# Optimization experiments

Measured on AMD Instinct MI355X. Metric: run time of the kernel, lower is better.

Reference implementation:

```python
import jax, jax.numpy as jnp
import numpy as np

L, B, S, D, H, E = 3, 2, 2048, 1024, 16, 4
Dh = D // H  # 64
DF = E * D   # 4096


def _ln(x, g, b, eps=1e-5):
    m = jnp.mean(x, axis=-1, keepdims=True)
    v = jnp.mean(jnp.square(x - m), axis=-1, keepdims=True)
    return (x - m) * jax.lax.rsqrt(v + eps) * g + b


def setup_inputs() -> dict:
    key = jax.random.key(0)
    ks = jax.random.split(key, 12)
    s = 0.02
    f32 = jnp.float32
    return {
        "x":    jax.random.normal(ks[0], (B, S, D), f32),
        "Wq":   jax.random.normal(ks[1], (L, Dh, Dh), f32) * s,
        "Wk":   jax.random.normal(ks[2], (L, Dh, Dh), f32) * s,
        "Wv":   jax.random.normal(ks[3], (L, Dh, Dh), f32) * s,
        "Wo":   jax.random.normal(ks[4], (L, D, D), f32) * s,
        "bo":   jnp.zeros((L, D), f32),
        "ln1_g": jnp.ones((L, D), f32),
        "ln1_b": jnp.zeros((L, D), f32),
        "W1":   jax.random.normal(ks[5], (L, DF, D), f32) * s,
        "b1":   jnp.zeros((L, DF), f32),
        "W2":   jax.random.normal(ks[6], (L, D, DF), f32) * s,
        "b2":   jnp.zeros((L, D), f32),
        "ln2_g": jnp.ones((L, D), f32),
        "ln2_b": jnp.zeros((L, D), f32),
    }


def reference(x, Wq, Wk, Wv, Wo, bo, ln1_g, ln1_b, W1, b1, W2, b2, ln2_g, ln2_b):
    scale = 1.0 / np.sqrt(Dh).astype(np.float32)
    out = x
    for l in range(L):
        xh = out.reshape(B, S, H, Dh)
        # per-head Linear (shared 64x64 weight across heads), torch Linear: y = x @ W.T
        q = jnp.einsum('bshd,ed->bhse', xh, Wq[l])  # [B,H,S,Dh]
        k = jnp.einsum('bshd,ed->bhse', xh, Wk[l])
        v = jnp.einsum('bshd,ed->bhse', xh, Wv[l])
        att = jax.nn.softmax(jnp.einsum('bhse,bhte->bhst', q, k) * scale, axis=-1)
        ctx = jnp.einsum('bhst,bhtd->bshd', att, v).reshape(B, S, D)
        att_out = ctx @ Wo[l].T + bo[l]
        n1 = _ln(att_out + out, ln1_g[l], ln1_b[l])  # residual adds layer input (v == out)
        ff = jax.nn.relu(n1 @ W1[l].T + b1[l]) @ W2[l].T + b2[l]
        out = _ln(ff + n1, ln2_g[l], ln2_b[l])
    return out
```

## Files before the change

kernel.cpp:

```cpp
#include <hip/hip_runtime.h>
#include <hip/hip_bf16.h>
#include <math.h>


#define DEVINL __device__ __forceinline__
typedef unsigned short ushort_t;
using short8 = __attribute__((ext_vector_type(8))) short;
using f32x4  = __attribute__((ext_vector_type(4))) float;

#if defined(__has_builtin)
#if __has_builtin(__builtin_amdgcn_exp2f)
#define EXPFN(x) __builtin_amdgcn_exp2f(x)
#define QSCALE 0.18033688011112042f
#define HAVE_EXP2 1
#endif
#endif
#ifndef HAVE_EXP2
#define EXPFN(x) __expf(x)
#define QSCALE 0.125f
#endif

DEVINL short f2b(float f) {
  unsigned u = __float_as_uint(f);
  u += 0x7fff + ((u >> 16) & 1);
  return (short)(u >> 16);
}
DEVINL unsigned pk2(float a, float b) {
  unsigned ua = __float_as_uint(a), ub = __float_as_uint(b);
  ua += 0x7fff + ((ua >> 16) & 1);
  ub += 0x7fff + ((ub >> 16) & 1);
  return (ua >> 16) | (ub & 0xffff0000u);
}
DEVINL unsigned pkc(float a, float b) {
  float2 f; f.x = a; f.y = b;
  __hip_bfloat162 h = __float22bfloat162_rn(f);
  return *reinterpret_cast<unsigned*>(&h);
}
DEVINL float bl(unsigned u) { return __uint_as_float(u << 16); }
DEVINL float bh(unsigned u) { return __uint_as_float(u & 0xffff0000u); }
DEVINL f32x4 mfma16(short8 a, short8 b, f32x4 c) {
  return __builtin_amdgcn_mfma_f32_16x16x32_bf16(a, b, c, 0, 0, 0);
}

typedef __attribute__((address_space(3))) void lds_void;
typedef __attribute__((address_space(1))) void gbl_void;
DEVINL void gl16(const void* g, void* l) {
  __builtin_amdgcn_global_load_lds((const gbl_void*)(unsigned long long)g,
                                   (lds_void*)(unsigned long long)l, 16, 0, 0);
}
template <int N> DEVINL void waitvm() {
  asm volatile("s_waitcnt vmcnt(%0)" ::"n"(N) : "memory");
}
DEVINL void barrier_raw() { __builtin_amdgcn_s_barrier(); }
DEVINL void sched0() { __builtin_amdgcn_sched_barrier(0); }

__global__ __launch_bounds__(256)
void conv_bf16(const float* __restrict__ src, ushort_t* __restrict__ dst,
               int n8) {
  int i = blockIdx.x * 256 + threadIdx.x;
  const int stride = gridDim.x * 256;
  for (; i < n8; i += stride) {
    float4 a = ((const float4*)src)[2 * i];
    float4 b = ((const float4*)src)[2 * i + 1];
    uint4 o;
    o.x = pk2(a.x, a.y); o.y = pk2(a.z, a.w);
    o.z = pk2(b.x, b.y); o.w = pk2(b.z, b.w);
    ((uint4*)dst)[i] = o;
  }
}

DEVINL float block_sum(float v, float* red) {
#pragma unroll
  for (int off = 32; off > 0; off >>= 1) v += __shfl_xor(v, off, 64);
  if ((threadIdx.x & 63) == 0) red[threadIdx.x >> 6] = v;
  __syncthreads();
  float r = red[0] + red[1] + red[2] + red[3];
  __syncthreads();
  return r;
}

template <bool WF>
__global__ __launch_bounds__(256)
void ln_fuse(const ushort_t* __restrict__ pa, const ushort_t* __restrict__ pb,
             const float* __restrict__ bias, const ushort_t* __restrict__ Rb,
             const float* __restrict__ g, const float* __restrict__ b,
             ushort_t* __restrict__ outb, float* __restrict__ outf) {
  __shared__ float red[4];
  const size_t base = (size_t)blockIdx.x * 1024 + threadIdx.x * 4;
  uint2 ua = *(const uint2*)(pa + base);
  uint2 ub = *(const uint2*)(pb + base);
  uint2 ur = *(const uint2*)(Rb + base);
  float4 vbi = *(const float4*)(bias + threadIdx.x * 4);
  float4 v;
  v.x = bl(ua.x) + bl(ub.x) + bl(ur.x) + vbi.x;
  v.y = bh(ua.x) + bh(ub.x) + bh(ur.x) + vbi.y;
  v.z = bl(ua.y) + bl(ub.y) + bl(ur.y) + vbi.z;
  v.w = bh(ua.y) + bh(ub.y) + bh(ur.y) + vbi.w;
  float s = block_sum(v.x + v.y + v.z + v.w, red);
  float mean = s * (1.0f / 1024.0f);
  float dx = v.x - mean, dy = v.y - mean, dz = v.z - mean, dw = v.w - mean;
  float sq = block_sum(dx * dx + dy * dy + dz * dz + dw * dw, red);
  float rstd = rsqrtf(sq * (1.0f / 1024.0f) + 1e-5f);
  const float4 gv = *(const float4*)(g + threadIdx.x * 4);
  const float4 bv = *(const float4*)(b + threadIdx.x * 4);
  float4 o;
  o.x = dx * rstd * gv.x + bv.x;
  o.y = dy * rstd * gv.y + bv.y;
  o.z = dz * rstd * gv.z + bv.z;
  o.w = dw * rstd * gv.w + bv.w;
  uint2 p;
  p.x = pk2(o.x, o.y); p.y = pk2(o.z, o.w);
  *(uint2*)(outb + base) = p;
  if (WF) *(float4*)(outf + base) = o;
}

template <int BM, int BN, int WR, int WC, bool OBF, int EPI, bool SWZ>
__global__ __launch_bounds__(WR * WC * 64)
void gemm_db(const ushort_t* __restrict__ A, const ushort_t* __restrict__ W,
             const float* __restrict__ bias, void* __restrict__ Cp, int M,
             int N, int Klen, int lda, int ldw) {
  constexpr int THREADS = WR * WC * 64;
  constexpr int FM = BM / WR / 16;
  constexpr int FN = BN / WC / 16;
  constexpr int CA = BM * 8 / THREADS;
  constexpr int CB = BN * 8 / THREADS;
  constexpr int L = CA + CB;
  __shared__ __align__(16) ushort_t As[2][BM * 64];
  __shared__ __align__(16) ushort_t Bs[2][BN * 64];
  const int tid = threadIdx.x;
  const int lane = tid & 63, lo = lane & 15, hi = lane >> 4, w = tid >> 6;
  int bx = blockIdx.x, by = blockIdx.y;
  if (SWZ) {
    int id = by * gridDim.x + bx;
    const int cpx = (gridDim.x * gridDim.y) >> 3;
    id = (id & 7) * cpx + (id >> 3);
    bx = id % gridDim.x;
    by = id / gridDim.x;
  }
  const int m0 = by * BM, n0 = bx * BN;
  const int wm = (w / WC) * (BM / WR), wn = (w % WC) * (BN / WC);
  const int kbase = blockIdx.z * Klen;

  auto stage = [&](int t, int buf) {
    const int k0 = kbase + t * 64;
#pragma unroll
    for (int i = 0; i < CA; ++i) {
      const int c = i * THREADS + tid;
      const int r = c >> 3, sg = (c & 7) ^ (r & 7);
      gl16(A + (size_t)(m0 + r) * lda + k0 + sg * 8, &As[buf][c * 8]);
    }
#pragma unroll
    for (int i = 0; i < CB; ++i) {
      const int c = i * THREADS + tid;
      const int r = c >> 3, sg = (c & 7) ^ (r & 7);
      gl16(W + (size_t)(n0 + r) * ldw + k0 + sg * 8, &Bs[buf][c * 8]);
    }
  };

  f32x4 acc[FM][FN] = {};
  auto compute = [&](int cur) {
#pragma unroll
    for (int ks = 0; ks < 2; ++ks) {
      short8 af[FM], bf_[FN];
#pragma unroll
      for (int fm = 0; fm < FM; ++fm) {
        const int row = wm + fm * 16 + lo;
        af[fm] = *(const short8*)
            &As[cur][row * 64 + (((ks * 4 + hi) ^ (row & 7)) << 3)];
      }
#pragma unroll
      for (int fn = 0; fn < FN; ++fn) {
        const int row = wn + fn * 16 + lo;
        bf_[fn] = *(const short8*)
            &Bs[cur][row * 64 + (((ks * 4 + hi) ^ (row & 7)) << 3)];
      }
#pragma unroll
      for (int fm = 0; fm < FM; ++fm)
#pragma unroll
        for (int fn = 0; fn < FN; ++fn)
          acc[fm][fn] = mfma16(af[fm], bf_[fn], acc[fm][fn]);
    }
  };

  const int nt = Klen / 64;
  stage(0, 0);
  for (int t = 0; t < nt - 1; ++t) {
    const int cur = t & 1;
    stage(t + 1, cur ^ 1);
    waitvm<L>();
    barrier_raw(); sched0();
    compute(cur);
    barrier_raw(); sched0();
  }
  waitvm<0>();
  barrier_raw(); sched0();
  compute((nt - 1) & 1);

  float bv[FN];
#pragma unroll
  for (int fn = 0; fn < FN; ++fn)
    bv[fn] = (EPI & 1) ? bias[n0 + wn + fn * 16 + lo] : 0.f;
#pragma unroll
  for (int fm = 0; fm < FM; ++fm)
#pragma unroll
    for (int fn = 0; fn < FN; ++fn) {
      const int col = n0 + wn + fn * 16 + lo;
#pragma unroll
      for (int r = 0; r < 4; ++r) {
        const int row = m0 + wm + fm * 16 + hi * 4 + r;
        float v = acc[fm][fn][r] + bv[fn];
        if (EPI & 4) v = fmaxf(v, 0.f);
        if (OBF) {
          ushort_t* Cb = (ushort_t*)Cp + (size_t)blockIdx.z * M * N;
          Cb[(size_t)row * N + col] = (ushort_t)f2b(v);
        } else {
          float* Cf = (float*)Cp + (size_t)blockIdx.z * M * N;
          Cf[(size_t)row * N + col] = v;
        }
      }
    }
}

__global__ __launch_bounds__(256)
void qkv_kernel(const ushort_t* __restrict__ A, const ushort_t* __restrict__ Wq,
                const ushort_t* __restrict__ Wk, const ushort_t* __restrict__ Wv,
                ushort_t* __restrict__ q, ushort_t* __restrict__ k,
                ushort_t* __restrict__ v) {
  __shared__ __align__(16) ushort_t As[128 * 64];
  __shared__ __align__(16) ushort_t Ws[3][64 * 64];
  const int tid = threadIdx.x;
  const int lane = tid & 63, lo = lane & 15, hi = lane >> 4, w = tid >> 6;
  const int m0 = blockIdx.x * 128;
  const int wm = (w >> 1) * 64, wn = (w & 1) * 32;

#pragma unroll
  for (int i = 0; i < 4; ++i) {
    const int c = i * 256 + tid;
    const int r = c >> 3, sg = (c & 7) ^ (r & 7);
    gl16(A + (size_t)(m0 + r) * 64 + sg * 8, As + c * 8);
  }
#pragma unroll
  for (int o = 0; o < 3; ++o) {
    const ushort_t* wb = (o == 0) ? Wq : (o == 1) ? Wk : Wv;
#pragma unroll
    for (int i = 0; i < 2; ++i) {
      const int c = i * 256 + tid;
      const int r = c >> 3, sg = (c & 7) ^ (r & 7);
      gl16(wb + (size_t)r * 64 + sg * 8, Ws[o] + c * 8);
    }
  }
  __syncthreads();

#pragma unroll
  for (int o = 0; o < 3; ++o) {
    ushort_t* ob = (o == 0) ? q : (o == 1) ? k : v;
    const float sc = (o == 0) ? QSCALE : 1.0f;
    f32x4 acc[4][2] = {};
#pragma unroll
    for (int ks = 0; ks < 2; ++ks) {
      short8 af[4], bf[2];
#pragma unroll
      for (int fm = 0; fm < 4; ++fm) {
        const int row = wm + fm * 16 + lo;
        af[fm] = *(const short8*)
            &As[row * 64 + (((ks * 4 + hi) ^ (row & 7)) << 3)];
      }
#pragma unroll
      for (int fn = 0; fn < 2; ++fn) {
        const int row = wn + fn * 16 + lo;
        bf[fn] = *(const short8*)
            &Ws[o][row * 64 + (((ks * 4 + hi) ^ (row & 7)) << 3)];
      }
#pragma unroll
      for (int fm = 0; fm < 4; ++fm)
#pragma unroll
        for (int fn = 0; fn < 2; ++fn)
          acc[fm][fn] = mfma16(af[fm], bf[fn], acc[fm][fn]);
    }
#pragma unroll
    for (int fm = 0; fm < 4; ++fm)
#pragma unroll
      for (int fn = 0; fn < 2; ++fn) {
        const int col = wn + fn * 16 + lo;
#pragma unroll
        for (int r = 0; r < 4; ++r) {
          const int row = m0 + wm + fm * 16 + hi * 4 + r;
          size_t idx;
          if (o == 2) {
            idx = (size_t)row * 64 + col;
          } else {
            idx = (size_t)((row >> 15) * 16 + (row & 15)) * 131072 +
                  (size_t)((row >> 4) & 2047) * 64 + col;
          }
          ob[idx] = (ushort_t)f2b(acc[fm][fn][r] * sc);
        }
      }
  }
}

__global__ __launch_bounds__(256)
void vtrans(const ushort_t* __restrict__ V, ushort_t* __restrict__ VT) {
  __shared__ ushort_t T[64][65];
  const int tid = threadIdx.x;
  const int s0 = blockIdx.x * 64, hd0 = blockIdx.y * 64, b = blockIdx.z;
  const ushort_t* src = V + (size_t)b * 2097152;
  ushort_t* dst = VT + (size_t)b * 2097152;
#pragma unroll
  for (int i = 0; i < 2; ++i) {
    int c = tid + i * 256;
    int s = c >> 3, kg = c & 7;
    short8 hv = *(const short8*)(src + (size_t)(s0 + s) * 1024 + hd0 + kg * 8);
#pragma unroll
    for (int j = 0; j < 8; ++j) T[s][kg * 8 + j] = (ushort_t)hv[j];
  }
  __syncthreads();
#pragma unroll
  for (int i = 0; i < 2; ++i) {
    int c = tid + i * 256;
    int hd = c >> 3, sg = c & 7;
    short8 o;
#pragma unroll
    for (int j = 0; j < 8; ++j) o[j] = (short)T[sg * 8 + j][hd];
    *(short8*)(dst + (size_t)(hd0 + hd) * 2048 + s0 + sg * 8) = o;
  }
}

__global__ __launch_bounds__(256)
void attn3(const ushort_t* __restrict__ Qh, const ushort_t* __restrict__ Kh,
           const ushort_t* __restrict__ VT, ushort_t* __restrict__ O) {
  __shared__ __align__(16) ushort_t Kbuf[2][64 * 64];
  __shared__ __align__(16) ushort_t Vbuf[2][64 * 64];
  __shared__ __align__(16) ushort_t Pbuf[4][16 * 40];
  const int tid = threadIdx.x, w = tid >> 6, lane = tid & 63;
  const int lo = lane & 15, hi = lane >> 4;
  const int hid = blockIdx.y * 32 + blockIdx.x;
  const int logical = (hid & 7) * 128 + (hid >> 3);
  const int bh = logical >> 5, qt = logical & 31;
  const int b = bh >> 4, h = bh & 15;
  const size_t hq = (size_t)bh * 131072;
  const size_t vth = (size_t)b * 2097152 + (size_t)h * 131072;
  const size_t oh = (size_t)b * 2097152 + (size_t)h * 64;
  const int qrow = qt * 64 + w * 16;
  ushort_t* Pw = Pbuf[w];

  const ushort_t* qp = Qh + hq + (size_t)(qrow + lo) * 64 + hi * 8;
  const short8 qf0 = *(const short8*)qp;
  const short8 qf1 = *(const short8*)(qp + 32);

  const int c0 = tid, c1 = 256 + tid;
  const int r0 = c0 >> 3, s0 = ((c0 & 7) ^ (r0 & 7)) << 3;
  const int r1 = c1 >> 3, s1 = ((c1 & 7) ^ (r1 & 7)) << 3;
  const ushort_t* kg0 = Kh + hq + (size_t)r0 * 64 + s0;
  const ushort_t* kg1 = Kh + hq + (size_t)r1 * 64 + s1;
  const ushort_t* vg0 = VT + vth + (size_t)r0 * 2048 + s0;
  const ushort_t* vg1 = VT + vth + (size_t)r1 * 2048 + s1;

  auto stage = [&](int kt, int buf) {
    gl16(kg0 + (size_t)kt * 4096, &Kbuf[buf][c0 * 8]);
    gl16(kg1 + (size_t)kt * 4096, &Kbuf[buf][c1 * 8]);
    gl16(vg0 + kt * 64, &Vbuf[buf][c0 * 8]);
    gl16(vg1 + kt * 64, &Vbuf[buf][c1 * 8]);
  };

  f32x4 acc[4] = {};
  f32x4 lacc = {};
  const int sw = lo & 7;
  const int ko0 = (hi ^ sw) << 3, ko1 = ((4 + hi) ^ sw) << 3;

  auto body = [&](const ushort_t* Kc, const ushort_t* Vc) {
    f32x4 sc[4];
#pragma unroll
    for (int fm = 0; fm < 4; ++fm) {
      const int rb = (fm * 16 + lo) * 64;
      f32x4 t = {};
      t = mfma16(*(const short8*)&Kc[rb + ko0], qf0, t);
      t = mfma16(*(const short8*)&Kc[rb + ko1], qf1, t);
      sc[fm] = t;
    }
    short8 vf[4][2];
#pragma unroll
    for (int fn = 0; fn < 4; ++fn) {
      const int rb = (fn * 16 + lo) * 64;
      vf[fn][0] = *(const short8*)&Vc[rb + ko0];
      vf[fn][1] = *(const short8*)&Vc[rb + ko1];
    }
#pragma unroll
    for (int fm = 0; fm < 4; ++fm) {
      f32x4 p;
      p[0] = EXPFN(sc[fm][0]); p[1] = EXPFN(sc[fm][1]);
      p[2] = EXPFN(sc[fm][2]); p[3] = EXPFN(sc[fm][3]);
      lacc += p;
      uint2 pw;
      pw.x = pkc(p[0], p[1]); pw.y = pkc(p[2], p[3]);
      *(uint2*)&Pw[lo * 40 + fm * 16 + hi * 4] = pw;
    }
    short8 pb0 = *(const short8*)&Pw[lo * 40 + hi * 8];
    short8 pb1 = *(const short8*)&Pw[lo * 40 + 32 + hi * 8];
#pragma unroll
    for (int fn = 0; fn < 4; ++fn) {
      acc[fn] = mfma16(vf[fn][0], pb0, acc[fn]);
      acc[fn] = mfma16(vf[fn][1], pb1, acc[fn]);
    }
  };

  stage(0, 0);
  __syncthreads();
  for (int kt2 = 0; kt2 < 16; ++kt2) {
    stage(2 * kt2 + 1, 1);
    body(Kbuf[0], Vbuf[0]);
    __syncthreads();
    if (kt2 < 15) stage(2 * kt2 + 2, 0);
    body(Kbuf[1], Vbuf[1]);
    __syncthreads();
  }

  float lsum = (lacc[0] + lacc[1]) + (lacc[2] + lacc[3]);
  lsum += __shfl_xor(lsum, 16);
  lsum += __shfl_xor(lsum, 32);
  const float inv = 1.0f / lsum;
  ushort_t* op = O + oh + (size_t)(qrow + lo) * 1024 + hi * 4;
#pragma unroll
  for (int fn = 0; fn < 4; ++fn) {
    uint2 o;
    o.x = pk2(acc[fn][0] * inv, acc[fn][1] * inv);
    o.y = pk2(acc[fn][2] * inv, acc[fn][3] * inv);
    *(uint2*)(op + fn * 16) = o;
  }
}

extern "C" void kernel_launch(void* const* d_in, const int* in_sizes, int n_in,
                              void* d_out, int out_size, void* d_ws,
                              size_t ws_size, hipStream_t stream) {
  const float* x    = (const float*)d_in[0];
  const float* Wq   = (const float*)d_in[1];
  const float* Wk   = (const float*)d_in[2];
  const float* Wv   = (const float*)d_in[3];
  const float* Wo   = (const float*)d_in[4];
  const float* bo   = (const float*)d_in[5];
  const float* ln1g = (const float*)d_in[6];
  const float* ln1b = (const float*)d_in[7];
  const float* W1   = (const float*)d_in[8];
  const float* b1   = (const float*)d_in[9];
  const float* W2   = (const float*)d_in[10];
  const float* b2   = (const float*)d_in[11];
  const float* ln2g = (const float*)d_in[12];
  const float* ln2b = (const float*)d_in[13];
  float* out = (float*)d_out;
  char* wsb = (char*)d_ws;

  ushort_t* t0  = (ushort_t*)wsb;
  ushort_t* t0b = t0 + 4194304;
  ushort_t* q   = (ushort_t*)(wsb + (16ull << 20));
  ushort_t* k   = (ushort_t*)(wsb + (24ull << 20));
  ushort_t* v   = (ushort_t*)(wsb + (32ull << 20));
  ushort_t* vt  = (ushort_t*)(wsb + (40ull << 20));
  ushort_t* ff  = q;
  ushort_t* ctx = (ushort_t*)(wsb + (48ull << 20));
  ushort_t* n1b = ctx;
  ushort_t* xbf = (ushort_t*)(wsb + (56ull << 20));
  ushort_t* wqb = (ushort_t*)(wsb + (64ull << 20));
  ushort_t* wkb = wqb + 3 * 4096;
  ushort_t* wvb = wkb + 3 * 4096;
  ushort_t* wob = (ushort_t*)(wsb + (65ull << 20));
  ushort_t* w1b = (ushort_t*)(wsb + (72ull << 20));
  ushort_t* w2b = (ushort_t*)(wsb + (96ull << 20));

  auto conv = [&](const float* s, ushort_t* d, long n) {
    int n8 = (int)(n / 8);
    int g = (n8 + 255) / 256;
    if (g > 2048) g = 2048;
    conv_bf16<<<g, 256, 0, stream>>>(s, d, n8);
  };
  conv(x, xbf, 4194304);
  conv(Wq, wqb, 3 * 4096);
  conv(Wk, wkb, 3 * 4096);
  conv(Wv, wvb, 3 * 4096);
  conv(Wo, wob, 3ll * 1048576);
  conv(W1, w1b, 3ll * 4194304);
  conv(W2, w2b, 3ll * 4194304);

  const ushort_t* curb = xbf;
  for (int l = 0; l < 3; ++l) {
    qkv_kernel<<<512, 256, 0, stream>>>(curb, wqb + l * 4096, wkb + l * 4096,
                                        wvb + l * 4096, q, k, v);
    vtrans<<<dim3(32, 16, 2), 256, 0, stream>>>(v, vt);
    attn3<<<dim3(32, 32), 256, 0, stream>>>(q, k, vt, ctx);
    gemm_db<128, 64, 2, 2, true, 0, true>
        <<<dim3(16, 32, 2), 256, 0, stream>>>(ctx, wob + (size_t)l * 1048576,
                                              nullptr, t0, 4096, 1024, 512,
                                              1024, 1024);
    ln_fuse<false><<<4096, 256, 0, stream>>>(t0, t0b, bo + l * 1024, curb,
                                             ln1g + l * 1024, ln1b + l * 1024,
                                             n1b, nullptr);
    gemm_db<128, 128, 2, 4, true, 5, true>
        <<<dim3(32, 32, 1), 512, 0, stream>>>(n1b, w1b + (size_t)l * 4194304,
                                              b1 + l * 4096, ff, 4096, 4096,
                                              1024, 1024, 1024);
    gemm_db<128, 64, 2, 2, true, 0, true>
        <<<dim3(16, 32, 2), 256, 0, stream>>>(ff, w2b + (size_t)l * 4194304,
                                              nullptr, t0, 4096, 1024, 2048,
                                              4096, 4096);
    if (l == 2)
      ln_fuse<true><<<4096, 256, 0, stream>>>(t0, t0b, b2 + l * 1024, n1b,
                                              ln2g + l * 1024, ln2b + l * 1024,
                                              xbf, out);
    else
      ln_fuse<false><<<4096, 256, 0, stream>>>(t0, t0b, b2 + l * 1024, n1b,
                                               ln2g + l * 1024, ln2b + l * 1024,
                                               xbf, nullptr);
    curb = xbf;
  }
}
```

Before: 611.8 us.

## Double attention query rows per warp and enlarge GEMM tiles

The attention kernel now processes 32 query rows per warp (128 per block) instead of 16, so each K/V tile loaded into LDS and each K fragment read serves two query blocks, halving K/V traffic per query. The grid shrinks to 16x32 blocks. The output-projection and FFN2 GEMMs switch to 128x128 tiles, and the FFN1 GEMM drops to a 2x2 warp layout with 256 threads. More accumulators per warp raise register pressure and fewer blocks may reduce occupancy.

Result: faster. 541.2 us (-11.5%).

```diff
diff --git a/kernel.cpp b/kernel.cpp
--- a/kernel.cpp
+++ b/kernel.cpp
@@ -326,26 +326,29 @@
 }
 
 __global__ __launch_bounds__(256)
-void attn3(const ushort_t* __restrict__ Qh, const ushort_t* __restrict__ Kh,
+void attn4(const ushort_t* __restrict__ Qh, const ushort_t* __restrict__ Kh,
            const ushort_t* __restrict__ VT, ushort_t* __restrict__ O) {
   __shared__ __align__(16) ushort_t Kbuf[2][64 * 64];
   __shared__ __align__(16) ushort_t Vbuf[2][64 * 64];
-  __shared__ __align__(16) ushort_t Pbuf[4][16 * 40];
+  __shared__ __align__(16) ushort_t Pbuf[4][2][16 * 40];
   const int tid = threadIdx.x, w = tid >> 6, lane = tid & 63;
   const int lo = lane & 15, hi = lane >> 4;
-  const int hid = blockIdx.y * 32 + blockIdx.x;
-  const int logical = (hid & 7) * 128 + (hid >> 3);
-  const int bh = logical >> 5, qt = logical & 31;
+  const int hid = blockIdx.y * 16 + blockIdx.x;
+  const int logical = (hid & 7) * 64 + (hid >> 3);
+  const int bh = logical >> 4, qt = logical & 15;
   const int b = bh >> 4, h = bh & 15;
   const size_t hq = (size_t)bh * 131072;
   const size_t vth = (size_t)b * 2097152 + (size_t)h * 131072;
   const size_t oh = (size_t)b * 2097152 + (size_t)h * 64;
-  const int qrow = qt * 64 + w * 16;
-  ushort_t* Pw = Pbuf[w];
-
-  const ushort_t* qp = Qh + hq + (size_t)(qrow + lo) * 64 + hi * 8;
-  const short8 qf0 = *(const short8*)qp;
-  const short8 qf1 = *(const short8*)(qp + 32);
+  const int qrow = qt * 128 + w * 32;
+  ushort_t* Pa = Pbuf[w][0];
+  ushort_t* Pb = Pbuf[w][1];
+
+  const ushort_t* qpa = Qh + hq + (size_t)(qrow + lo) * 64 + hi * 8;
+  const short8 qf0a = *(const short8*)qpa;
+  const short8 qf1a = *(const short8*)(qpa + 32);
+  const short8 qf0b = *(const short8*)(qpa + 1024);
+  const short8 qf1b = *(const short8*)(qpa + 1024 + 32);
 
   const int c0 = tid, c1 = 256 + tid;
   const int r0 = c0 >> 3, s0 = ((c0 & 7) ^ (r0 & 7)) << 3;
@@ -362,20 +365,26 @@
     gl16(vg1 + kt * 64, &Vbuf[buf][c1 * 8]);
   };
 
-  f32x4 acc[4] = {};
-  f32x4 lacc = {};
+  f32x4 acca[4] = {}, accb[4] = {};
+  f32x4 la = {}, lb = {};
   const int sw = lo & 7;
   const int ko0 = (hi ^ sw) << 3, ko1 = ((4 + hi) ^ sw) << 3;
 
   auto body = [&](const ushort_t* Kc, const ushort_t* Vc) {
-    f32x4 sc[4];
+    f32x4 sa[4], sb[4];
 #pragma unroll
     for (int fm = 0; fm < 4; ++fm) {
       const int rb = (fm * 16 + lo) * 64;
-      f32x4 t = {};
-      t = mfma16(*(const short8*)&Kc[rb + ko0], qf0, t);
-      t = mfma16(*(const short8*)&Kc[rb + ko1], qf1, t);
-      sc[fm] = t;
+      short8 k0 = *(const short8*)&Kc[rb + ko0];
+      short8 k1 = *(const short8*)&Kc[rb + ko1];
+      f32x4 ta = {};
+      ta = mfma16(k0, qf0a, ta);
+      ta = mfma16(k1, qf1a, ta);
+      sa[fm] = ta;
+      f32x4 tb = {};
+      tb = mfma16(k0, qf0b, tb);
+      tb = mfma16(k1, qf1b, tb);
+      sb[fm] = tb;
     }
     short8 vf[4][2];
 #pragma unroll
@@ -387,19 +396,30 @@
 #pragma unroll
     for (int fm = 0; fm < 4; ++fm) {
       f32x4 p;
-      p[0] = EXPFN(sc[fm][0]); p[1] = EXPFN(sc[fm][1]);
-      p[2] = EXPFN(sc[fm][2]); p[3] = EXPFN(sc[fm][3]);
-      lacc += p;
+      p[0] = EXPFN(sa[fm][0]); p[1] = EXPFN(sa[fm][1]);
+      p[2] = EXPFN(sa[fm][2]); p[3] = EXPFN(sa[fm][3]);
+      la += p;
       uint2 pw;
       pw.x = pkc(p[0], p[1]); pw.y = pkc(p[2], p[3]);
-      *(uint2*)&Pw[lo * 40 + fm * 16 + hi * 4] = pw;
-    }
-    short8 pb0 = *(const short8*)&Pw[lo * 40 + hi * 8];
-    short8 pb1 = *(const short8*)&Pw[lo * 40 + 32 + hi * 8];
+      *(uint2*)&Pa[lo * 40 + fm * 16 + hi * 4] = pw;
+      f32x4 r;
+      r[0] = EXPFN(sb[fm][0]); r[1] = EXPFN(sb[fm][1]);
+      r[2] = EXPFN(sb[fm][2]); r[3] = EXPFN(sb[fm][3]);
+      lb += r;
+      uint2 rw;
+      rw.x = pkc(r[0], r[1]); rw.y = pkc(r[2], r[3]);
+      *(uint2*)&Pb[lo * 40 + fm * 16 + hi * 4] = rw;
+    }
+    short8 pa0 = *(const short8*)&Pa[lo * 40 + hi * 8];
+    short8 pa1 = *(const short8*)&Pa[lo * 40 + 32 + hi * 8];
+    short8 pb0 = *(const short8*)&Pb[lo * 40 + hi * 8];
+    short8 pb1 = *(const short8*)&Pb[lo * 40 + 32 + hi * 8];
 #pragma unroll
     for (int fn = 0; fn < 4; ++fn) {
-      acc[fn] = mfma16(vf[fn][0], pb0, acc[fn]);
-      acc[fn] = mfma16(vf[fn][1], pb1, acc[fn]);
+      acca[fn] = mfma16(vf[fn][0], pa0, acca[fn]);
+      acca[fn] = mfma16(vf[fn][1], pa1, acca[fn]);
+      accb[fn] = mfma16(vf[fn][0], pb0, accb[fn]);
+      accb[fn] = mfma16(vf[fn][1], pb1, accb[fn]);
     }
   };
 
@@ -414,17 +434,24 @@
     __syncthreads();
   }
 
-  float lsum = (lacc[0] + lacc[1]) + (lacc[2] + lacc[3]);
-  lsum += __shfl_xor(lsum, 16);
-  lsum += __shfl_xor(lsum, 32);
-  const float inv = 1.0f / lsum;
-  ushort_t* op = O + oh + (size_t)(qrow + lo) * 1024 + hi * 4;
+  float lsa = (la[0] + la[1]) + (la[2] + la[3]);
+  lsa += __shfl_xor(lsa, 16);
+  lsa += __shfl_xor(lsa, 32);
+  float lsb = (lb[0] + lb[1]) + (lb[2] + lb[3]);
+  lsb += __shfl_xor(lsb, 16);
+  lsb += __shfl_xor(lsb, 32);
+  const float inva = 1.0f / lsa, invb = 1.0f / lsb;
+  ushort_t* opa = O + oh + (size_t)(qrow + lo) * 1024 + hi * 4;
+  ushort_t* opb = opa + 16 * 1024;
 #pragma unroll
   for (int fn = 0; fn < 4; ++fn) {
-    uint2 o;
-    o.x = pk2(acc[fn][0] * inv, acc[fn][1] * inv);
-    o.y = pk2(acc[fn][2] * inv, acc[fn][3] * inv);
-    *(uint2*)(op + fn * 16) = o;
+    uint2 oa, ob;
+    oa.x = pk2(acca[fn][0] * inva, acca[fn][1] * inva);
+    oa.y = pk2(acca[fn][2] * inva, acca[fn][3] * inva);
+    ob.x = pk2(accb[fn][0] * invb, accb[fn][1] * invb);
+    ob.y = pk2(accb[fn][2] * invb, accb[fn][3] * invb);
+    *(uint2*)(opa + fn * 16) = oa;
+    *(uint2*)(opb + fn * 16) = ob;
   }
 }
 
@@ -484,22 +511,22 @@
     qkv_kernel<<<512, 256, 0, stream>>>(curb, wqb + l * 4096, wkb + l * 4096,
                                         wvb + l * 4096, q, k, v);
     vtrans<<<dim3(32, 16, 2), 256, 0, stream>>>(v, vt);
-    attn3<<<dim3(32, 32), 256, 0, stream>>>(q, k, vt, ctx);
-    gemm_db<128, 64, 2, 2, true, 0, true>
-        <<<dim3(16, 32, 2), 256, 0, stream>>>(ctx, wob + (size_t)l * 1048576,
-                                              nullptr, t0, 4096, 1024, 512,
-                                              1024, 1024);
+    attn4<<<dim3(16, 32), 256, 0, stream>>>(q, k, vt, ctx);
+    gemm_db<128, 128, 2, 2, true, 0, true>
+        <<<dim3(8, 32, 2), 256, 0, stream>>>(ctx, wob + (size_t)l * 1048576,
+                                             nullptr, t0, 4096, 1024, 512,
+                                             1024, 1024);
     ln_fuse<false><<<4096, 256, 0, stream>>>(t0, t0b, bo + l * 1024, curb,
                                              ln1g + l * 1024, ln1b + l * 1024,
                                              n1b, nullptr);
-    gemm_db<128, 128, 2, 4, true, 5, true>
-        <<<dim3(32, 32, 1), 512, 0, stream>>>(n1b, w1b + (size_t)l * 4194304,
+    gemm_db<128, 128, 2, 2, true, 5, true>
+        <<<dim3(32, 32, 1), 256, 0, stream>>>(n1b, w1b + (size_t)l * 4194304,
                                               b1 + l * 4096, ff, 4096, 4096,
                                               1024, 1024, 1024);
-    gemm_db<128, 64, 2, 2, true, 0, true>
-        <<<dim3(16, 32, 2), 256, 0, stream>>>(ff, w2b + (size_t)l * 4194304,
-                                              nullptr, t0, 4096, 1024, 2048,
-                                              4096, 4096);
+    gemm_db<128, 128, 2, 2, true, 0, true>
+        <<<dim3(8, 32, 2), 256, 0, stream>>>(ff, w2b + (size_t)l * 4194304,
+                                             nullptr, t0, 4096, 1024, 2048,
+                                             4096, 4096);
     if (l == 2)
       ln_fuse<true><<<4096, 256, 0, stream>>>(t0, t0b, b2 + l * 1024, n1b,
                                               ln2g + l * 1024, ln2b + l * 1024,
```
